# Optimization experiments

Measured on AMD Instinct MI355X. Metric: run time of the kernel, lower is better.

The kernel has to match this reference:

```python
import jax, jax.numpy as jnp
import numpy as np
from jax.ops import segment_sum

N_NODES = 100000
N_EDGES = 3200000
DIM = 256
N_CLASSES = 32
N_GRAPHS = 64


def setup_inputs() -> dict:
    key = jax.random.key(0)
    k1, k2, k3, k4, k5 = jax.random.split(key, 5)
    x = jax.random.normal(k1, (N_NODES, DIM), dtype=jnp.float32)
    W = jax.random.normal(k2, (DIM, N_CLASSES), dtype=jnp.float32) / np.sqrt(DIM)
    b = jax.random.normal(k3, (N_CLASSES,), dtype=jnp.float32) * 0.01
    edge_index = jax.random.randint(k4, (2, N_EDGES), 0, N_NODES, dtype=jnp.int64)
    batch = jnp.sort(jax.random.randint(k5, (N_NODES,), 0, N_GRAPHS, dtype=jnp.int64))
    return {"x": x, "W": W, "b": b, "edge_index": edge_index, "batch": batch}


def reference(x, W, b, edge_index, batch):
    N = x.shape[0]
    # GCNConv: linear transform (no bias), then normalized aggregation, then bias
    h = x @ W  # [N, C]
    # add self loops (PyG default add_self_loops=True)
    loop = jnp.arange(N, dtype=edge_index.dtype)
    src = jnp.concatenate([edge_index[0], loop])  # source (message sender)
    dst = jnp.concatenate([edge_index[1], loop])  # target (aggregation site)
    # symmetric normalization: deg computed at target with unit edge weights
    deg = segment_sum(jnp.ones_like(dst, dtype=h.dtype), dst, num_segments=N)
    dinv = jnp.where(deg > 0, jax.lax.rsqrt(deg), 0.0)
    norm = dinv[src] * dinv[dst]  # [E+N]
    msg = h[src] * norm[:, None]  # gather + scale
    out = segment_sum(msg, dst, num_segments=N) + b  # scatter-add, bias after agg
    # global_mean_pool: segment mean over graphs
    cnt = segment_sum(jnp.ones((N,), dtype=out.dtype), batch, num_segments=N_GRAPHS)
    sums = segment_sum(out, batch, num_segments=N_GRAPHS)
    return sums / jnp.maximum(cnt, 1.0)[:, None]
```

## Files before the change

### kernel.cpp

```cpp
#include <hip/hip_runtime.h>

#define NN    100000
#define NE    3200000
#define DIMK  256
#define NC    32
#define NG    64

#define ROWS   128
#define NBUCK  782
#define CAP    4608
#define NB1    512
#define EPB    6250
#define NSL    16
#define MAXG   512

static constexpr size_t OFF_REC    = 0;
static constexpr size_t OFF_DINV   = 14417920;
static constexpr size_t OFF_BTOT   = 14817920;
static constexpr size_t OFF_START  = 14821120;
static constexpr size_t OFF_CTRL   = 14821504;
static constexpr size_t OFF_P2     = 14821632;
static constexpr size_t OFF_PART   = 15870208;
static constexpr size_t OFF_DEGARR = OFF_PART;
static constexpr size_t OFF_CNT    = OFF_PART + 400000;
static constexpr size_t OFF_EXC    = OFF_PART + 2001536;

__device__ __forceinline__ int idx_at(const void* p, long i, bool i64) {
    return i64 ? (int)((const long long*)p)[i] : ((const int*)p)[i];
}

__global__ void k_detect(const int* __restrict__ ei_raw, int* __restrict__ ctrl) {
    int z = (ei_raw[1] == 0) + (ei_raw[3] == 0) + (ei_raw[5] == 0) +
            (ei_raw[7] == 0) + (ei_raw[9] == 0) + (ei_raw[11] == 0);
    ctrl[0] = (z == 6) ? 1 : 0;
    ctrl[1] = 0;
}

__global__ __launch_bounds__(256) void k_pre(const void* __restrict__ ei,
        unsigned int* __restrict__ parts, int* __restrict__ cnt,
        const int* __restrict__ ctrl) {
    __shared__ unsigned int h[12500];
    const bool i64 = ctrl[0] != 0;
    const int b = blockIdx.x;
    if (b < 256) {
        const int hh = b >> 7;
        const int sl = b & 127;
        const int lo = hh * 50000, hi = lo + 50000;
        for (int t = threadIdx.x; t < 12500; t += 256) h[t] = 0u;
        __syncthreads();
        const int e0 = sl * 25000;
        for (int e = e0 + threadIdx.x; e < e0 + 25000; e += 256) {
            int d = idx_at(ei, (long)NE + e, i64);
            if (d >= lo && d < hi) {
                int r = d - lo;
                atomicAdd(&h[r >> 2], 1u << ((r & 3) * 8));
            }
        }
        __syncthreads();
        for (int t = threadIdx.x; t < 12500; t += 256)
            parts[(size_t)b * 12500 + t] = h[t];
    } else {
        const int k = b - 256;
        for (int t = threadIdx.x; t < NBUCK; t += 256) h[t] = 0u;
        __syncthreads();
        const int e0 = k * EPB;
        for (int e = e0 + threadIdx.x; e < e0 + EPB; e += 256) {
            int s = idx_at(ei, e, i64);
            atomicAdd(&h[s >> 7], 1u);
        }
        __syncthreads();
        for (int t = threadIdx.x; t < NBUCK; t += 256)
            cnt[t * NB1 + k] = (int)h[t];
    }
}

__global__ __launch_bounds__(512) void k_mid(const unsigned int* __restrict__ parts,
        unsigned int* __restrict__ degarr, float* __restrict__ dinv,
        const void* __restrict__ batch, int* __restrict__ start,
        const int* __restrict__ cnt, int* __restrict__ exc, int* __restrict__ btot,
        const int* __restrict__ ctrl) {
    __shared__ int s[512];
    const int b = blockIdx.x;
    const int t = threadIdx.x;
    if (b < 49) {
        int i = b * 512 + t;
        if (i >= 25000) return;
        int h = (i >= 12500) ? 1 : 0;
        int w = i - h * 12500;
        int c0 = 0, c1 = 0, c2 = 0, c3 = 0;
        const unsigned int* base = parts + (size_t)(h * 128) * 12500 + w;
#pragma unroll 4
        for (int q = 0; q < 128; ++q) {
            unsigned int v = base[(size_t)q * 12500];
            c0 += v & 255u; c1 += (v >> 8) & 255u; c2 += (v >> 16) & 255u; c3 += v >> 24;
        }
        int node = h * 50000 + w * 4;
        degarr[node]     = 1u + c0;  dinv[node]     = 1.0f / sqrtf((float)(1 + c0));
        degarr[node + 1] = 1u + c1;  dinv[node + 1] = 1.0f / sqrtf((float)(1 + c1));
        degarr[node + 2] = 1u + c2;  dinv[node + 2] = 1.0f / sqrtf((float)(1 + c2));
        degarr[node + 3] = 1u + c3;  dinv[node + 3] = 1.0f / sqrtf((float)(1 + c3));
    } else if (b < 245) {
        const bool i64 = ctrl[0] != 0;
        int i = (b - 49) * 512 + t;
        if (i >= NN) return;
        int bi = idx_at(batch, i, i64);
        int bp = (i == 0) ? -1 : idx_at(batch, i - 1, i64);
        for (int g = bp + 1; g <= bi; ++g) start[g] = i;
        if (i == NN - 1)
            for (int g = bi + 1; g <= NG; ++g) start[g] = NN;
    } else {
        const int bkt = b - 245;
        int v = cnt[bkt * NB1 + t];
        s[t] = v;
        __syncthreads();
        for (int off = 1; off < 512; off <<= 1) {
            int u = (t >= off) ? s[t - off] : 0;
            __syncthreads();
            s[t] += u;
            __syncthreads();
        }
        exc[bkt * NB1 + t] = bkt * CAP + (s[t] - v);
        if (t == 511) btot[bkt] = s[511];
    }
}

__global__ __launch_bounds__(256) void k_place(const void* __restrict__ ei,
        const void* __restrict__ batch, const unsigned int* __restrict__ degarr,
        const int* __restrict__ exc, unsigned int* __restrict__ rec,
        const int* __restrict__ ctrl) {
    __shared__ unsigned int lc[NBUCK];
    __shared__ int lbase[NBUCK];
    const bool i64 = ctrl[0] != 0;
    const int k = blockIdx.x;
    for (int t = threadIdx.x; t < NBUCK; t += 256) {
        lc[t] = 0u;
        lbase[t] = exc[t * NB1 + k];
    }
    __syncthreads();
    const int e0 = k * EPB;
    for (int e = e0 + threadIdx.x; e < e0 + EPB; e += 256) {
        int s = idx_at(ei, e, i64);
        int d = idx_at(ei, (long)NE + e, i64);
        int g = idx_at(batch, d, i64);
        unsigned int deg = min(degarr[d], 524287u);
        int b = s >> 7;
        unsigned int r = atomicAdd(&lc[b], 1u);
        rec[lbase[b] + (int)r] = (deg << 13) | (unsigned)((s & 127) * 64 + g);
    }
}

__global__ __launch_bounds__(512, 4) void k_fused(
        const float* __restrict__ x, const float* __restrict__ dinv,
        const void* __restrict__ batch, const unsigned int* __restrict__ rec,
        const int* __restrict__ btot, float* __restrict__ part,
        int* __restrict__ ctrl) {
    __shared__ __align__(16) float Ach[ROWS * 64];
    __shared__ __align__(16) float xs[16][DIMK];
    __shared__ int sbkt;
    const bool i64 = ctrl[0] != 0;
    const int tid = threadIdx.x;
    const int gi = tid >> 6;
    const int di = tid & 63;

    float acc[8][4];
#pragma unroll
    for (int g = 0; g < 8; ++g)
#pragma unroll
        for (int k = 0; k < 4; ++k) acc[g][k] = 0.0f;

    const float4* x4 = (const float4*)x;

    for (;;) {
        if (tid == 0) sbkt = atomicAdd(&ctrl[1], 1);
        __syncthreads();
        const int bkt = sbkt;
        if (bkt >= NBUCK) break;
        const int j0 = bkt * ROWS;
        const int j1 = min(j0 + ROWS, NN);

        for (int t = tid; t < ROWS * 64; t += 512) Ach[t] = 0.0f;
        __syncthreads();
        if (tid < ROWS) {
            int j = j0 + tid;
            if (j < NN) Ach[tid * 64 + idx_at(batch, j, i64)] = dinv[j];
        }
        __syncthreads();
        const int rb = bkt * CAP;
        const int re = rb + btot[bkt];
        for (int r = rb + tid; r < re; r += 512) {
            unsigned int q = rec[r];
            float val = 1.0f / sqrtf((float)(q >> 13));
            atomicAdd(&Ach[q & 8191u], val);
        }
        __syncthreads();

        for (int c0 = 0; c0 < ROWS; c0 += 16) {
            for (int t = tid; t < 16 * 64; t += 512) {
                int jj = t >> 6, d4 = t & 63;
                int j = j0 + c0 + jj;
                float4 v = make_float4(0.f, 0.f, 0.f, 0.f);
                if (j < j1) {
                    float dv = dinv[j];
                    float4 w = x4[(size_t)j * 64 + d4];
                    v.x = dv * w.x; v.y = dv * w.y; v.z = dv * w.z; v.w = dv * w.w;
                }
                ((float4*)xs[jj])[d4] = v;
            }
            __syncthreads();
#pragma unroll
            for (int jj = 0; jj < 16; ++jj) {
                const float* arow = Ach + (c0 + jj) * 64 + gi * 8;
                float4 p0 = *(const float4*)arow;
                float4 p1 = *(const float4*)(arow + 4);
                float4 xv = ((const float4*)xs[jj])[di];
                float pg[8] = {p0.x, p0.y, p0.z, p0.w, p1.x, p1.y, p1.z, p1.w};
#pragma unroll
                for (int g = 0; g < 8; ++g) {
                    acc[g][0] = fmaf(pg[g], xv.x, acc[g][0]);
                    acc[g][1] = fmaf(pg[g], xv.y, acc[g][1]);
                    acc[g][2] = fmaf(pg[g], xv.z, acc[g][2]);
                    acc[g][3] = fmaf(pg[g], xv.w, acc[g][3]);
                }
            }
            __syncthreads();
        }
    }

    float* p = part + (size_t)blockIdx.x * (NG * DIMK);
#pragma unroll
    for (int g = 0; g < 8; ++g) {
        float4 w = make_float4(acc[g][0], acc[g][1], acc[g][2], acc[g][3]);
        ((float4*)(p + (gi * 8 + g) * DIMK))[di] = w;
    }
}

__global__ __launch_bounds__(256) void k_reduce1(const float4* __restrict__ part,
        float4* __restrict__ p2, int nblk) {
    int id = blockIdx.x * 256 + threadIdx.x;
    int c4 = id & 4095;
    int sl = id >> 12;
    int span = (nblk + NSL - 1) / NSL;
    int b0 = sl * span, b1 = min(b0 + span, nblk);
    float4 s = make_float4(0.f, 0.f, 0.f, 0.f);
    for (int b = b0; b < b1; ++b) {
        float4 v = part[(size_t)b * 4096 + c4];
        s.x += v.x; s.y += v.y; s.z += v.z; s.w += v.w;
    }
    p2[(size_t)sl * 4096 + c4] = s;
}

__global__ __launch_bounds__(256) void k_final(const float* __restrict__ p2,
        const float* __restrict__ W, const float* __restrict__ bias,
        const int* __restrict__ start, float* __restrict__ out) {
    __shared__ float Sb[8 * DIMK];
    const int tid = threadIdx.x, b = blockIdx.x;
    for (int t = tid; t < 8 * DIMK; t += 256) {
        int gl = t >> 8, d = t & 255;
        float s = 0.f;
#pragma unroll
        for (int sl = 0; sl < NSL; ++sl)
            s += p2[(size_t)sl * (NG * DIMK) + (b * 8 + gl) * DIMK + d];
        Sb[t] = s;
    }
    __syncthreads();
    int g = tid >> 5, c = tid & 31;
    float sum = 0.f;
#pragma unroll 8
    for (int d = 0; d < DIMK; ++d)
        sum = fmaf(Sb[g * DIMK + d], W[d * NC + c], sum);
    int gg = b * 8 + g;
    float cn = (float)max(start[gg + 1] - start[gg], 1);
    out[gg * NC + c] = sum / cn + bias[c];
}

extern "C" void kernel_launch(void* const* d_in, const int* in_sizes, int n_in,
                              void* d_out, int out_size, void* d_ws, size_t ws_size,
                              hipStream_t stream) {
    const float* x    = (const float*)d_in[0];
    const float* W    = (const float*)d_in[1];
    const float* bias = (const float*)d_in[2];
    const void*  ei   = d_in[3];
    const void*  batch= d_in[4];
    float* out = (float*)d_out;

    char* ws = (char*)d_ws;
    unsigned int* rec  = (unsigned int*)(ws + OFF_REC);
    unsigned int* degp = (unsigned int*)(ws + OFF_REC);
    float* dinv  = (float*)(ws + OFF_DINV);
    int*   btot  = (int*)(ws + OFF_BTOT);
    int*   start = (int*)(ws + OFF_START);
    int*   ctrl  = (int*)(ws + OFF_CTRL);
    float* p2    = (float*)(ws + OFF_P2);
    float* part  = (float*)(ws + OFF_PART);
    unsigned int* degarr = (unsigned int*)(ws + OFF_DEGARR);
    int*   cnt   = (int*)(ws + OFF_CNT);
    int*   exc   = (int*)(ws + OFF_EXC);

    long avail = (long)(ws_size - OFF_PART) / 65536;
    int grid = (int)avail;
    if (grid > MAXG) grid = MAXG;
    if (grid < 64) grid = 64;

    k_detect <<<1, 1, 0, stream>>>((const int*)ei, ctrl);
    k_pre    <<<768, 256, 0, stream>>>(ei, degp, cnt, ctrl);
    k_mid    <<<1027, 512, 0, stream>>>(degp, degarr, dinv, batch, start,
                                        cnt, exc, btot, ctrl);
    k_place  <<<NB1, 256, 0, stream>>>(ei, batch, degarr, exc, rec, ctrl);
    k_fused  <<<grid, 512, 0, stream>>>(x, dinv, batch, rec, btot, part, ctrl);
    k_reduce1<<<256, 256, 0, stream>>>((const float4*)part, (float4*)p2, grid);
    k_final  <<<8, 256, 0, stream>>>(p2, W, bias, start, out);
}
```

Measured before the change: 220.0 us.

## Inline dtype detection, register-prefetch x tiles, fold dinv into adjacency

Drops the single-thread detect kernel by recomputing the int64 check inline in each kernel, and moves the ctrl counter reset into k_place. In the fused kernel, x rows are prefetched into registers one 16-row chunk ahead so global loads overlap the FMA loop. The per-row dinv scaling moves off the x tile and onto the adjacency block. The maximum grid rises to 768. This saves a launch and hides load latency, at the cost of more registers and an extra sync per chunk.

```diff
diff --git a/kernel.cpp b/kernel.cpp
--- a/kernel.cpp
+++ b/kernel.cpp
@@ -12,7 +12,7 @@
 #define NB1    512
 #define EPB    6250
 #define NSL    16
-#define MAXG   512
+#define MAXG   768
 
 static constexpr size_t OFF_REC    = 0;
 static constexpr size_t OFF_DINV   = 14417920;
@@ -29,18 +29,16 @@
     return i64 ? (int)((const long long*)p)[i] : ((const int*)p)[i];
 }
 
-__global__ void k_detect(const int* __restrict__ ei_raw, int* __restrict__ ctrl) {
-    int z = (ei_raw[1] == 0) + (ei_raw[3] == 0) + (ei_raw[5] == 0) +
-            (ei_raw[7] == 0) + (ei_raw[9] == 0) + (ei_raw[11] == 0);
-    ctrl[0] = (z == 6) ? 1 : 0;
-    ctrl[1] = 0;
+__device__ __forceinline__ bool detect_i64(const void* ei) {
+    const int* w = (const int*)ei;
+    return (w[1] == 0) & (w[3] == 0) & (w[5] == 0) &
+           (w[7] == 0) & (w[9] == 0) & (w[11] == 0);
 }
 
 __global__ __launch_bounds__(256) void k_pre(const void* __restrict__ ei,
-        unsigned int* __restrict__ parts, int* __restrict__ cnt,
-        const int* __restrict__ ctrl) {
+        unsigned int* __restrict__ parts, int* __restrict__ cnt) {
     __shared__ unsigned int h[12500];
-    const bool i64 = ctrl[0] != 0;
+    const bool i64 = detect_i64(ei);
     const int b = blockIdx.x;
     if (b < 256) {
         const int hh = b >> 7;
@@ -76,9 +74,9 @@
 
 __global__ __launch_bounds__(512) void k_mid(const unsigned int* __restrict__ parts,
         unsigned int* __restrict__ degarr, float* __restrict__ dinv,
-        const void* __restrict__ batch, int* __restrict__ start,
-        const int* __restrict__ cnt, int* __restrict__ exc, int* __restrict__ btot,
-        const int* __restrict__ ctrl) {
+        const void* __restrict__ batch, const void* __restrict__ ei,
+        int* __restrict__ start, const int* __restrict__ cnt,
+        int* __restrict__ exc, int* __restrict__ btot) {
     __shared__ int s[512];
     const int b = blockIdx.x;
     const int t = threadIdx.x;
@@ -100,7 +98,7 @@
         degarr[node + 2] = 1u + c2;  dinv[node + 2] = 1.0f / sqrtf((float)(1 + c2));
         degarr[node + 3] = 1u + c3;  dinv[node + 3] = 1.0f / sqrtf((float)(1 + c3));
     } else if (b < 245) {
-        const bool i64 = ctrl[0] != 0;
+        const bool i64 = detect_i64(ei);
         int i = (b - 49) * 512 + t;
         if (i >= NN) return;
         int bi = idx_at(batch, i, i64);
@@ -127,11 +125,12 @@
 __global__ __launch_bounds__(256) void k_place(const void* __restrict__ ei,
         const void* __restrict__ batch, const unsigned int* __restrict__ degarr,
         const int* __restrict__ exc, unsigned int* __restrict__ rec,
-        const int* __restrict__ ctrl) {
+        int* __restrict__ ctrl) {
     __shared__ unsigned int lc[NBUCK];
     __shared__ int lbase[NBUCK];
-    const bool i64 = ctrl[0] != 0;
+    const bool i64 = detect_i64(ei);
     const int k = blockIdx.x;
+    if (k == 0 && threadIdx.x == 0) ctrl[1] = 0;
     for (int t = threadIdx.x; t < NBUCK; t += 256) {
         lc[t] = 0u;
         lbase[t] = exc[t * NB1 + k];
@@ -151,13 +150,14 @@
 
 __global__ __launch_bounds__(512, 4) void k_fused(
         const float* __restrict__ x, const float* __restrict__ dinv,
-        const void* __restrict__ batch, const unsigned int* __restrict__ rec,
-        const int* __restrict__ btot, float* __restrict__ part,
-        int* __restrict__ ctrl) {
+        const void* __restrict__ batch, const void* __restrict__ ei,
+        const unsigned int* __restrict__ rec, const int* __restrict__ btot,
+        float* __restrict__ part, int* __restrict__ ctrl) {
     __shared__ __align__(16) float Ach[ROWS * 64];
-    __shared__ __align__(16) float xs[16][DIMK];
+    __shared__ __align__(16) float4 xs4[16 * 64];
+    __shared__ float dinvs[ROWS];
     __shared__ int sbkt;
-    const bool i64 = ctrl[0] != 0;
+    const bool i64 = detect_i64(ei);
     const int tid = threadIdx.x;
     const int gi = tid >> 6;
     const int di = tid & 63;
@@ -169,50 +169,70 @@
         for (int k = 0; k < 4; ++k) acc[g][k] = 0.0f;
 
     const float4* x4 = (const float4*)x;
+    const float4 z4 = make_float4(0.f, 0.f, 0.f, 0.f);
+    float4* Ach4 = (float4*)Ach;
+    float4 pf0, pf1;
+    int j0 = 0, j1 = 0;
 
     for (;;) {
         if (tid == 0) sbkt = atomicAdd(&ctrl[1], 1);
         __syncthreads();
         const int bkt = sbkt;
         if (bkt >= NBUCK) break;
-        const int j0 = bkt * ROWS;
-        const int j1 = min(j0 + ROWS, NN);
-
-        for (int t = tid; t < ROWS * 64; t += 512) Ach[t] = 0.0f;
+        j0 = bkt * ROWS;
+        j1 = min(j0 + ROWS, NN);
+
+        {
+            int jA = j0 + (tid >> 6), jB = j0 + ((tid + 512) >> 6);
+            pf0 = (jA < j1) ? x4[(size_t)jA * 64 + (tid & 63)] : z4;
+            pf1 = (jB < j1) ? x4[(size_t)jB * 64 + ((tid + 512) & 63)] : z4;
+        }
+#pragma unroll
+        for (int k = 0; k < 4; ++k) Ach4[tid + 512 * k] = z4;
         __syncthreads();
         if (tid < ROWS) {
             int j = j0 + tid;
-            if (j < NN) Ach[tid * 64 + idx_at(batch, j, i64)] = dinv[j];
-        }
-        __syncthreads();
-        const int rb = bkt * CAP;
-        const int re = rb + btot[bkt];
-        for (int r = rb + tid; r < re; r += 512) {
-            unsigned int q = rec[r];
-            float val = 1.0f / sqrtf((float)(q >> 13));
-            atomicAdd(&Ach[q & 8191u], val);
-        }
+            float v = 0.f;
+            if (j < j1) {
+                v = dinv[j];
+                Ach[tid * 64 + idx_at(batch, j, i64)] = v;
+            }
+            dinvs[tid] = v;
+        }
+        __syncthreads();
+        {
+            const int rb = bkt * CAP;
+            const int re = rb + btot[bkt];
+            for (int r = rb + tid; r < re; r += 512) {
+                unsigned int q = rec[r];
+                float val = 1.0f / sqrtf((float)(q >> 13));
+                atomicAdd(&Ach[q & 8191u], val);
+            }
+        }
+        __syncthreads();
+#pragma unroll
+        for (int k = 0; k < 16; ++k) {
+            int e = tid + 512 * k;
+            Ach[e] *= dinvs[e >> 6];
+        }
+        xs4[tid] = pf0;
+        xs4[tid + 512] = pf1;
         __syncthreads();
 
         for (int c0 = 0; c0 < ROWS; c0 += 16) {
-            for (int t = tid; t < 16 * 64; t += 512) {
-                int jj = t >> 6, d4 = t & 63;
-                int j = j0 + c0 + jj;
-                float4 v = make_float4(0.f, 0.f, 0.f, 0.f);
-                if (j < j1) {
-                    float dv = dinv[j];
-                    float4 w = x4[(size_t)j * 64 + d4];
-                    v.x = dv * w.x; v.y = dv * w.y; v.z = dv * w.z; v.w = dv * w.w;
-                }
-                ((float4*)xs[jj])[d4] = v;
-            }
-            __syncthreads();
+            const bool more = (c0 + 16 < ROWS);
+            if (more) {
+                int ib = c0 + 16;
+                int jA = j0 + ib + (tid >> 6), jB = j0 + ib + ((tid + 512) >> 6);
+                pf0 = (jA < j1) ? x4[(size_t)jA * 64 + (tid & 63)] : z4;
+                pf1 = (jB < j1) ? x4[(size_t)jB * 64 + ((tid + 512) & 63)] : z4;
+            }
 #pragma unroll
             for (int jj = 0; jj < 16; ++jj) {
                 const float* arow = Ach + (c0 + jj) * 64 + gi * 8;
                 float4 p0 = *(const float4*)arow;
                 float4 p1 = *(const float4*)(arow + 4);
-                float4 xv = ((const float4*)xs[jj])[di];
+                float4 xv = xs4[jj * 64 + di];
                 float pg[8] = {p0.x, p0.y, p0.z, p0.w, p1.x, p1.y, p1.z, p1.w};
 #pragma unroll
                 for (int g = 0; g < 8; ++g) {
@@ -223,6 +243,11 @@
                 }
             }
             __syncthreads();
+            if (more) {
+                xs4[tid] = pf0;
+                xs4[tid + 512] = pf1;
+                __syncthreads();
+            }
         }
     }
 
@@ -301,12 +326,11 @@
     if (grid > MAXG) grid = MAXG;
     if (grid < 64) grid = 64;
 
-    k_detect <<<1, 1, 0, stream>>>((const int*)ei, ctrl);
-    k_pre    <<<768, 256, 0, stream>>>(ei, degp, cnt, ctrl);
-    k_mid    <<<1027, 512, 0, stream>>>(degp, degarr, dinv, batch, start,
-                                        cnt, exc, btot, ctrl);
+    k_pre    <<<768, 256, 0, stream>>>(ei, degp, cnt);
+    k_mid    <<<1027, 512, 0, stream>>>(degp, degarr, dinv, batch, ei, start,
+                                        cnt, exc, btot);
     k_place  <<<NB1, 256, 0, stream>>>(ei, batch, degarr, exc, rec, ctrl);
-    k_fused  <<<grid, 512, 0, stream>>>(x, dinv, batch, rec, btot, part, ctrl);
+    k_fused  <<<grid, 512, 0, stream>>>(x, dinv, batch, ei, rec, btot, part, ctrl);
     k_reduce1<<<256, 256, 0, stream>>>((const float4*)part, (float4*)p2, grid);
     k_final  <<<8, 256, 0, stream>>>(p2, W, bias, start, out);
 }
```

Result: slower. 813.1 us (+269.5%).
